# Optimization experiments

Measured on AMD Instinct MI355X. Metric: run time of the kernel, lower is better.

Reference implementation:

```python
import jax, jax.numpy as jnp
import numpy as np

N_NODES = 100000
N_EDGES = 1600000
IN_FEATS = 128
H_FEATS = 128


def setup_inputs() -> dict:
    key = jax.random.key(0)
    ks = jax.random.split(key, 8)
    s_in = 1.0 / np.sqrt(IN_FEATS)
    s_h = 1.0 / np.sqrt(H_FEATS)
    return {
        "emb_weight": jax.random.normal(ks[0], (N_NODES, IN_FEATS), jnp.float32),
        "W1_self": jax.random.normal(ks[1], (IN_FEATS, H_FEATS), jnp.float32) * s_in,
        "W1_neigh": jax.random.normal(ks[2], (IN_FEATS, H_FEATS), jnp.float32) * s_in,
        "b1": jnp.zeros((H_FEATS,), jnp.float32),
        "W2_self": jax.random.normal(ks[3], (H_FEATS, H_FEATS), jnp.float32) * s_h,
        "W2_neigh": jax.random.normal(ks[4], (H_FEATS, H_FEATS), jnp.float32) * s_h,
        "b2": jnp.zeros((H_FEATS,), jnp.float32),
        "edges": jax.random.randint(ks[5], (2, N_EDGES), 0, N_NODES, jnp.int64)
            if jax.config.jax_enable_x64 else
            jax.random.randint(ks[5], (2, N_EDGES), 0, N_NODES, jnp.int32),
    }


def _sage_conv(h, src, dst, W_self, W_neigh, b):
    # DGL SAGEConv(mean): out = h @ W_self + mean_neigh(h) @ W_neigh + b
    agg = jax.ops.segment_sum(h[src], dst, num_segments=N_NODES)  # [N, F]
    deg = jax.ops.segment_sum(jnp.ones((src.shape[0],), h.dtype), dst,
                              num_segments=N_NODES)
    mean = agg / jnp.maximum(deg, 1.0)[:, None]  # zero-in-degree -> zeros
    return h @ W_self + mean @ W_neigh + b


def reference(emb_weight, W1_self, W1_neigh, b1, W2_self, W2_neigh, b2, edges):
    src, dst = edges[0], edges[1]
    h = emb_weight  # node_emb(g.nodes()) over all nodes
    h = _sage_conv(h, src, dst, W1_self, W1_neigh, b1)
    h = jax.nn.leaky_relu(h, negative_slope=0.2)
    # dropout is identity in eval mode
    h = _sage_conv(h, src, dst, W2_self, W2_neigh, b2)
    return h
```

## Files before the change

kernel.cpp:

```cpp
#include <hip/hip_runtime.h>
#include <hip/hip_bf16.h>

#define N_NODES_C 100000
#define FEATS 128
#define SH 10
#define NBK 128
#define PB  256
#define CAST_BLOCKS 12500

typedef unsigned int uint32;
typedef __bf16 bf16_t;
typedef bf16_t bf16x8 __attribute__((ext_vector_type(8)));
typedef float f32x4 __attribute__((ext_vector_type(4)));

union Frag { uint4 u; bf16x8 v; };

__device__ __forceinline__ unsigned short f32_to_bf16_bits(float f) {
    uint32 u = __float_as_uint(f);
    u += 0x7fffu + ((u >> 16) & 1u);
    return (unsigned short)(u >> 16);
}
__device__ __forceinline__ float bf16_lo(uint32 p) { return __uint_as_float(p << 16); }
__device__ __forceinline__ float bf16_hi(uint32 p) { return __uint_as_float(p & 0xffff0000u); }

__global__ __launch_bounds__(256) void prep_fused(
    const int* __restrict__ dst, int* __restrict__ gHist, int nE, int chunk,
    const float4* __restrict__ emb4, unsigned short* __restrict__ hb0, int n4,
    const float* __restrict__ W1s, const float* __restrict__ W1n, unsigned short* __restrict__ wt1,
    const float* __restrict__ W2s, const float* __restrict__ W2n, unsigned short* __restrict__ wt2)
{
    __shared__ int h[NBK];
    const int b = blockIdx.x;
    const int tid = threadIdx.x;

    if (b < PB) {
        if (tid < NBK) h[tid] = 0;
        __syncthreads();
        const int b0 = b * chunk;
        const int e1 = min(b0 + chunk, nE);
        for (int e = b0 + tid; e < e1; e += 256)
            atomicAdd(&h[dst[e] >> SH], 1);
        __syncthreads();
        if (tid < NBK) gHist[tid * PB + b] = h[tid];
    } else if (b < PB + 32) {
        const int which = (b - PB) >> 4;
        const float* Ws = which ? W2s : W1s;
        const float* Wn = which ? W2n : W1n;
        unsigned short* wt = which ? wt2 : wt1;
        int gid = ((b - PB) & 15) * 256 + tid;
        int frag = gid >> 6, lane = gid & 63;
        int nt = frag >> 3, ks = frag & 7;
        int n = nt * 16 + (lane & 15);
        int kbase = ks * 32 + (lane >> 4) * 8;
        union { unsigned short s[8]; uint4 u; } o;
#pragma unroll
        for (int j = 0; j < 8; ++j) {
            int k = kbase + j;
            float v = (k < 128) ? Ws[(size_t)k * FEATS + n] : Wn[(size_t)(k - 128) * FEATS + n];
            o.s[j] = f32_to_bf16_bits(v);
        }
        *(uint4*)(wt + (size_t)gid * 8) = o.u;
    } else {
        int i = (b - PB - 32) * 256 + tid;
        if (i >= n4) return;
        float4 v = emb4[i];
        union { unsigned short s[4]; uint2 u; } o;
        o.s[0] = f32_to_bf16_bits(v.x);
        o.s[1] = f32_to_bf16_bits(v.y);
        o.s[2] = f32_to_bf16_bits(v.z);
        o.s[3] = f32_to_bf16_bits(v.w);
        *(uint2*)(hb0 + (size_t)i * 4) = o.u;
    }
}

__global__ __launch_bounds__(1024) void scan_one(int* __restrict__ g) {
    __shared__ int ss[1024];
    const int tid = threadIdx.x;
    const int base = tid * 32;
    int pref[32];
    int sum = 0;
#pragma unroll
    for (int j = 0; j < 32; ++j) {
        int v = g[base + j];
        pref[j] = sum;
        sum += v;
    }
    ss[tid] = sum;
    __syncthreads();
    for (int d = 1; d < 1024; d <<= 1) {
        int t = (tid >= d) ? ss[tid - d] : 0;
        __syncthreads();
        ss[tid] += t;
        __syncthreads();
    }
    int ex = ss[tid] - sum;
#pragma unroll
    for (int j = 0; j < 32; ++j)
        g[base + j] = ex + pref[j];
}

__global__ __launch_bounds__(1024) void part_scatter(const int* __restrict__ src,
                                                     const int* __restrict__ dst,
                                                     const int* __restrict__ gScan,
                                                     uint32* __restrict__ ebuf,
                                                     int nE, int chunk) {
    __shared__ int cur[NBK];
    const int tid = threadIdx.x;
    if (tid < NBK) cur[tid] = gScan[tid * PB + blockIdx.x];
    __syncthreads();
    const int b0 = blockIdx.x * chunk;
    const int e1 = min(b0 + chunk, nE);
    for (int e = b0 + tid; e < e1; e += 1024) {
        int d = dst[e];
        int pos = atomicAdd(&cur[d >> SH], 1);
        ebuf[pos] = (uint32)src[e] | ((uint32)(d & ((1 << SH) - 1)) << 17);
    }
}

__global__ __launch_bounds__(1024) void bucket_csr(const uint32* __restrict__ ebuf,
                                                   const int* __restrict__ gScan,
                                                   int* __restrict__ off,
                                                   int* __restrict__ csr,
                                                   int nE) {
    __shared__ int cnt[1 << SH];
    __shared__ int ss[1 << SH];
    const int b = blockIdx.x;
    const int tid = threadIdx.x;
    const int start = gScan[b * PB];
    const int end = gScan[(b + 1) * PB];
    const int nodeBase = b << SH;
    cnt[tid] = 0;
    __syncthreads();
    for (int e = start + tid; e < end; e += 1024)
        atomicAdd(&cnt[ebuf[e] >> 17], 1);
    __syncthreads();
    int own = cnt[tid];
    ss[tid] = own;
    __syncthreads();
    for (int d = 1; d < 1024; d <<= 1) {
        int t = (tid >= d) ? ss[tid - d] : 0;
        __syncthreads();
        ss[tid] += t;
        __syncthreads();
    }
    int ex = ss[tid] - own;
    cnt[tid] = ex;
    int node = nodeBase + tid;
    if (node < N_NODES_C) off[node] = start + ex;
    if (b == gridDim.x - 1 && tid == 0) off[N_NODES_C] = nE;
    __syncthreads();
    for (int e = start + tid; e < end; e += 1024) {
        uint32 p = ebuf[e];
        int pos = atomicAdd(&cnt[p >> 17], 1);
        csr[start + pos] = (int)((p & 0x1FFFFu) << 8);
    }
}

__global__ __launch_bounds__(256) void gather_mean_w2(const unsigned short* __restrict__ hb,
                                                      const int* __restrict__ csrB,
                                                      const int* __restrict__ off,
                                                      unsigned short* __restrict__ meanb,
                                                      int nNodes) {
    const int node = blockIdx.x * 4 + (threadIdx.x >> 6);
    const int lane = threadIdx.x & 63;
    if (node >= nNodes) return;
    const int start = __builtin_amdgcn_readfirstlane(off[node]);
    const int end   = __builtin_amdgcn_readfirstlane(off[node + 1]);
    const int half = lane >> 5;
    const int c = lane & 31;
    const char* base = (const char*)hb + (size_t)(c * 8);
    float a0 = 0.f, a1 = 0.f, a2 = 0.f, a3 = 0.f;
    int e = start;
    for (; e + 16 <= end; e += 16) {
        const int o0  = csrB[e + 0],  o1  = csrB[e + 1],  o2  = csrB[e + 2],  o3  = csrB[e + 3];
        const int o4  = csrB[e + 4],  o5  = csrB[e + 5],  o6  = csrB[e + 6],  o7  = csrB[e + 7];
        const int o8  = csrB[e + 8],  o9  = csrB[e + 9],  o10 = csrB[e + 10], o11 = csrB[e + 11];
        const int o12 = csrB[e + 12], o13 = csrB[e + 13], o14 = csrB[e + 14], o15 = csrB[e + 15];
        const uint2 u0 = *(const uint2*)(base + (size_t)(half ? o1  : o0));
        const uint2 u1 = *(const uint2*)(base + (size_t)(half ? o3  : o2));
        const uint2 u2 = *(const uint2*)(base + (size_t)(half ? o5  : o4));
        const uint2 u3 = *(const uint2*)(base + (size_t)(half ? o7  : o6));
        const uint2 u4 = *(const uint2*)(base + (size_t)(half ? o9  : o8));
        const uint2 u5 = *(const uint2*)(base + (size_t)(half ? o11 : o10));
        const uint2 u6 = *(const uint2*)(base + (size_t)(half ? o13 : o12));
        const uint2 u7 = *(const uint2*)(base + (size_t)(half ? o15 : o14));
        a0 += bf16_lo(u0.x); a1 += bf16_hi(u0.x); a2 += bf16_lo(u0.y); a3 += bf16_hi(u0.y);
        a0 += bf16_lo(u1.x); a1 += bf16_hi(u1.x); a2 += bf16_lo(u1.y); a3 += bf16_hi(u1.y);
        a0 += bf16_lo(u2.x); a1 += bf16_hi(u2.x); a2 += bf16_lo(u2.y); a3 += bf16_hi(u2.y);
        a0 += bf16_lo(u3.x); a1 += bf16_hi(u3.x); a2 += bf16_lo(u3.y); a3 += bf16_hi(u3.y);
        a0 += bf16_lo(u4.x); a1 += bf16_hi(u4.x); a2 += bf16_lo(u4.y); a3 += bf16_hi(u4.y);
        a0 += bf16_lo(u5.x); a1 += bf16_hi(u5.x); a2 += bf16_lo(u5.y); a3 += bf16_hi(u5.y);
        a0 += bf16_lo(u6.x); a1 += bf16_hi(u6.x); a2 += bf16_lo(u6.y); a3 += bf16_hi(u6.y);
        a0 += bf16_lo(u7.x); a1 += bf16_hi(u7.x); a2 += bf16_lo(u7.y); a3 += bf16_hi(u7.y);
    }
    if (e + 8 <= end) {
        const int o0 = csrB[e + 0], o1 = csrB[e + 1], o2 = csrB[e + 2], o3 = csrB[e + 3];
        const int o4 = csrB[e + 4], o5 = csrB[e + 5], o6 = csrB[e + 6], o7 = csrB[e + 7];
        const uint2 u0 = *(const uint2*)(base + (size_t)(half ? o1 : o0));
        const uint2 u1 = *(const uint2*)(base + (size_t)(half ? o3 : o2));
        const uint2 u2 = *(const uint2*)(base + (size_t)(half ? o5 : o4));
        const uint2 u3 = *(const uint2*)(base + (size_t)(half ? o7 : o6));
        a0 += bf16_lo(u0.x); a1 += bf16_hi(u0.x); a2 += bf16_lo(u0.y); a3 += bf16_hi(u0.y);
        a0 += bf16_lo(u1.x); a1 += bf16_hi(u1.x); a2 += bf16_lo(u1.y); a3 += bf16_hi(u1.y);
        a0 += bf16_lo(u2.x); a1 += bf16_hi(u2.x); a2 += bf16_lo(u2.y); a3 += bf16_hi(u2.y);
        a0 += bf16_lo(u3.x); a1 += bf16_hi(u3.x); a2 += bf16_lo(u3.y); a3 += bf16_hi(u3.y);
        e += 8;
    }
    if (e + 4 <= end) {
        const int o0 = csrB[e + 0], o1 = csrB[e + 1], o2 = csrB[e + 2], o3 = csrB[e + 3];
        const uint2 u0 = *(const uint2*)(base + (size_t)(half ? o1 : o0));
        const uint2 u1 = *(const uint2*)(base + (size_t)(half ? o3 : o2));
        a0 += bf16_lo(u0.x); a1 += bf16_hi(u0.x); a2 += bf16_lo(u0.y); a3 += bf16_hi(u0.y);
        a0 += bf16_lo(u1.x); a1 += bf16_hi(u1.x); a2 += bf16_lo(u1.y); a3 += bf16_hi(u1.y);
        e += 4;
    }
    if (e + 2 <= end) {
        const int o0 = csrB[e + 0], o1 = csrB[e + 1];
        const uint2 u = *(const uint2*)(base + (size_t)(half ? o1 : o0));
        a0 += bf16_lo(u.x); a1 += bf16_hi(u.x); a2 += bf16_lo(u.y); a3 += bf16_hi(u.y);
        e += 2;
    }
    if (e < end && half == 0) {
        const uint2 u = *(const uint2*)(base + (size_t)csrB[e]);
        a0 += bf16_lo(u.x); a1 += bf16_hi(u.x); a2 += bf16_lo(u.y); a3 += bf16_hi(u.y);
    }
    a0 += __shfl_xor(a0, 32);
    a1 += __shfl_xor(a1, 32);
    a2 += __shfl_xor(a2, 32);
    a3 += __shfl_xor(a3, 32);
    const int deg = end - start;
    const float invd = (deg > 0) ? (1.f / (float)deg) : 0.f;
    if (half == 0) {
        uint2 o;
        o.x = ((uint32)f32_to_bf16_bits(a1 * invd) << 16) | (uint32)f32_to_bf16_bits(a0 * invd);
        o.y = ((uint32)f32_to_bf16_bits(a3 * invd) << 16) | (uint32)f32_to_bf16_bits(a2 * invd);
        ((uint2*)meanb)[(size_t)node * 32 + c] = o;
    }
}

__global__ __launch_bounds__(256) void sage_gemm_mfma(const unsigned short* __restrict__ HB,
                                                      const unsigned short* __restrict__ MB,
                                                      const unsigned short* __restrict__ WT,
                                                      const float* __restrict__ bias,
                                                      void* __restrict__ OUTP,
                                                      int nNodes, int mode) {
    const int wave = threadIdx.x >> 6;
    const int lane = threadIdx.x & 63;
    const int waveBase = blockIdx.x * 64 + wave * 16;
    const int m = lane & 15;
    const int quad = lane >> 4;

    int arow = waveBase + m;
    if (arow >= nNodes) arow = nNodes - 1;
    const uint4* hrow = (const uint4*)(HB + (size_t)arow * FEATS);
    const uint4* mrow = (const uint4*)(MB + (size_t)arow * FEATS);

    Frag a[8];
#pragma unroll
    for (int ks = 0; ks < 4; ++ks) a[ks].u = hrow[ks * 4 + quad];
#pragma unroll
    for (int ks = 0; ks < 4; ++ks) a[ks + 4].u = mrow[ks * 4 + quad];

    const uint4* wt4 = (const uint4*)WT;
    f32x4 acc[8];
#pragma unroll
    for (int nt = 0; nt < 8; ++nt) acc[nt] = (f32x4){0.f, 0.f, 0.f, 0.f};

#pragma unroll
    for (int ks = 0; ks < 8; ++ks) {
#pragma unroll
        for (int nt = 0; nt < 8; ++nt) {
            Frag b;
            b.u = wt4[(size_t)(nt * 8 + ks) * 64 + lane];
            acc[nt] = __builtin_amdgcn_mfma_f32_16x16x32_bf16(a[ks].v, b.v, acc[nt], 0, 0, 0);
        }
    }

#pragma unroll
    for (int nt = 0; nt < 8; ++nt) {
        const int col = nt * 16 + m;
        const float bv = bias[col];
#pragma unroll
        for (int r = 0; r < 4; ++r) {
            const int grow = waveBase + quad * 4 + r;
            if (grow >= nNodes) continue;
            float v = acc[nt][r] + bv;
            if (mode) {
                v = v > 0.f ? v : 0.2f * v;
                ((unsigned short*)OUTP)[(size_t)grow * FEATS + col] = f32_to_bf16_bits(v);
            } else {
                ((float*)OUTP)[(size_t)grow * FEATS + col] = v;
            }
        }
    }
}

extern "C" void kernel_launch(void* const* d_in, const int* in_sizes, int n_in,
                              void* d_out, int out_size, void* d_ws, size_t ws_size,
                              hipStream_t stream) {
    const float* emb = (const float*)d_in[0];
    const float* W1s = (const float*)d_in[1];
    const float* W1n = (const float*)d_in[2];
    const float* b1  = (const float*)d_in[3];
    const float* W2s = (const float*)d_in[4];
    const float* W2n = (const float*)d_in[5];
    const float* b2  = (const float*)d_in[6];
    const int*   edg = (const int*)d_in[7];

    const int nE = in_sizes[7] / 2;
    const int* src = edg;
    const int* dst = edg + nE;

    const int chunk = (nE + PB - 1) / PB;
    const int nActB = (N_NODES_C + (1 << SH) - 1) >> SH;
    const int n4 = N_NODES_C * FEATS / 4;

    const size_t bfTab = (size_t)N_NODES_C * FEATS * sizeof(unsigned short);

    char* ws = (char*)d_ws;
    int* off      = (int*)(ws);
    int* gHist    = (int*)(ws + (512 << 10));
    int* csr      = (int*)(ws + (1 << 20));
    uint32* ebuf  = (uint32*)(ws + (8 << 20));
    unsigned short* wt1 = (unsigned short*)(ws + (15 << 20));
    unsigned short* wt2 = (unsigned short*)(ws + (15 << 20) + (64 << 10));
    unsigned short* hb0 = (unsigned short*)(ws + (16 << 20));
    unsigned short* h1b = (unsigned short*)((char*)hb0 + bfTab);
    unsigned short* mnb = (unsigned short*)((char*)h1b + bfTab);
    float* out = (float*)d_out;

    prep_fused<<<PB + 32 + CAST_BLOCKS, 256, 0, stream>>>(
        dst, gHist, nE, chunk, (const float4*)emb, hb0, n4,
        W1s, W1n, wt1, W2s, W2n, wt2);

    scan_one<<<1, 1024, 0, stream>>>(gHist);
    part_scatter<<<PB, 1024, 0, stream>>>(src, dst, gHist, ebuf, nE, chunk);
    bucket_csr<<<nActB, 1024, 0, stream>>>(ebuf, gHist, off, csr, nE);

    const int gatherBlocks = (N_NODES_C + 3) / 4;
    const int gemmBlocks = (N_NODES_C + 63) / 64;

    gather_mean_w2<<<gatherBlocks, 256, 0, stream>>>(hb0, csr, off, mnb, N_NODES_C);
    sage_gemm_mfma<<<gemmBlocks, 256, 0, stream>>>(hb0, mnb, wt1, b1, h1b, N_NODES_C, 1);

    gather_mean_w2<<<gatherBlocks, 256, 0, stream>>>(h1b, csr, off, mnb, N_NODES_C);
    sage_gemm_mfma<<<gemmBlocks, 256, 0, stream>>>(h1b, mnb, wt2, b2, out, N_NODES_C, 0);
}
```

Before: 336.1 us.

## Build CSR with per-node atomic counting and stage GEMM weights in LDS

```diff
diff --git a/kernel.cpp b/kernel.cpp
--- a/kernel.cpp
+++ b/kernel.cpp
@@ -3,8 +3,6 @@
 
 #define N_NODES_C 100000
 #define FEATS 128
-#define SH 10
-#define NBK 128
 #define PB  256
 #define CAST_BLOCKS 12500
 
@@ -24,24 +22,19 @@
 __device__ __forceinline__ float bf16_hi(uint32 p) { return __uint_as_float(p & 0xffff0000u); }
 
 __global__ __launch_bounds__(256) void prep_fused(
-    const int* __restrict__ dst, int* __restrict__ gHist, int nE, int chunk,
+    const int* __restrict__ dst, int* __restrict__ deg, int nE, int chunk,
     const float4* __restrict__ emb4, unsigned short* __restrict__ hb0, int n4,
     const float* __restrict__ W1s, const float* __restrict__ W1n, unsigned short* __restrict__ wt1,
     const float* __restrict__ W2s, const float* __restrict__ W2n, unsigned short* __restrict__ wt2)
 {
-    __shared__ int h[NBK];
     const int b = blockIdx.x;
     const int tid = threadIdx.x;
 
     if (b < PB) {
-        if (tid < NBK) h[tid] = 0;
-        __syncthreads();
         const int b0 = b * chunk;
         const int e1 = min(b0 + chunk, nE);
         for (int e = b0 + tid; e < e1; e += 256)
-            atomicAdd(&h[dst[e] >> SH], 1);
-        __syncthreads();
-        if (tid < NBK) gHist[tid * PB + b] = h[tid];
+            atomicAdd(&deg[dst[e]], 1);
     } else if (b < PB + 32) {
         const int which = (b - PB) >> 4;
         const float* Ws = which ? W2s : W1s;
@@ -73,18 +66,17 @@
     }
 }
 
-__global__ __launch_bounds__(1024) void scan_one(int* __restrict__ g) {
+__global__ __launch_bounds__(1024) void scan_nodes(const int* __restrict__ deg,
+                                                   int* __restrict__ off,
+                                                   int* __restrict__ cur,
+                                                   int nNodes, int nE) {
     __shared__ int ss[1024];
     const int tid = threadIdx.x;
-    const int base = tid * 32;
-    int pref[32];
+    const int per = (nNodes + 1023) >> 10;
+    const int lo = tid * per;
+    const int hi = min(lo + per, nNodes);
     int sum = 0;
-#pragma unroll
-    for (int j = 0; j < 32; ++j) {
-        int v = g[base + j];
-        pref[j] = sum;
-        sum += v;
-    }
+    for (int i = lo; i < hi; ++i) sum += deg[i];
     ss[tid] = sum;
     __syncthreads();
     for (int d = 1; d < 1024; d <<= 1) {
@@ -93,66 +85,25 @@
         ss[tid] += t;
         __syncthreads();
     }
-    int ex = ss[tid] - sum;
-#pragma unroll
-    for (int j = 0; j < 32; ++j)
-        g[base + j] = ex + pref[j];
-}
-
-__global__ __launch_bounds__(1024) void part_scatter(const int* __restrict__ src,
-                                                     const int* __restrict__ dst,
-                                                     const int* __restrict__ gScan,
-                                                     uint32* __restrict__ ebuf,
-                                                     int nE, int chunk) {
-    __shared__ int cur[NBK];
-    const int tid = threadIdx.x;
-    if (tid < NBK) cur[tid] = gScan[tid * PB + blockIdx.x];
-    __syncthreads();
-    const int b0 = blockIdx.x * chunk;
-    const int e1 = min(b0 + chunk, nE);
-    for (int e = b0 + tid; e < e1; e += 1024) {
-        int d = dst[e];
-        int pos = atomicAdd(&cur[d >> SH], 1);
-        ebuf[pos] = (uint32)src[e] | ((uint32)(d & ((1 << SH) - 1)) << 17);
-    }
-}
-
-__global__ __launch_bounds__(1024) void bucket_csr(const uint32* __restrict__ ebuf,
-                                                   const int* __restrict__ gScan,
-                                                   int* __restrict__ off,
+    int run = ss[tid] - sum;
+    for (int i = lo; i < hi; ++i) {
+        int d = deg[i];
+        off[i] = run;
+        cur[i] = run;
+        run += d;
+    }
+    if (tid == 0) off[nNodes] = nE;
+}
+
+__global__ __launch_bounds__(256) void place_edges(const int* __restrict__ src,
+                                                   const int* __restrict__ dst,
+                                                   int* __restrict__ cur,
                                                    int* __restrict__ csr,
                                                    int nE) {
-    __shared__ int cnt[1 << SH];
-    __shared__ int ss[1 << SH];
-    const int b = blockIdx.x;
-    const int tid = threadIdx.x;
-    const int start = gScan[b * PB];
-    const int end = gScan[(b + 1) * PB];
-    const int nodeBase = b << SH;
-    cnt[tid] = 0;
-    __syncthreads();
-    for (int e = start + tid; e < end; e += 1024)
-        atomicAdd(&cnt[ebuf[e] >> 17], 1);
-    __syncthreads();
-    int own = cnt[tid];
-    ss[tid] = own;
-    __syncthreads();
-    for (int d = 1; d < 1024; d <<= 1) {
-        int t = (tid >= d) ? ss[tid - d] : 0;
-        __syncthreads();
-        ss[tid] += t;
-        __syncthreads();
-    }
-    int ex = ss[tid] - own;
-    cnt[tid] = ex;
-    int node = nodeBase + tid;
-    if (node < N_NODES_C) off[node] = start + ex;
-    if (b == gridDim.x - 1 && tid == 0) off[N_NODES_C] = nE;
-    __syncthreads();
-    for (int e = start + tid; e < end; e += 1024) {
-        uint32 p = ebuf[e];
-        int pos = atomicAdd(&cnt[p >> 17], 1);
-        csr[start + pos] = (int)((p & 0x1FFFFu) << 8);
+    const int stride = gridDim.x * 256;
+    for (int e = blockIdx.x * 256 + threadIdx.x; e < nE; e += stride) {
+        int pos = atomicAdd(&cur[dst[e]], 1);
+        csr[pos] = src[e] << 8;
     }
 }
 
@@ -238,15 +189,22 @@
     }
 }
 
-__global__ __launch_bounds__(256) void sage_gemm_mfma(const unsigned short* __restrict__ HB,
+__global__ __launch_bounds__(512) void sage_gemm_mfma(const unsigned short* __restrict__ HB,
                                                       const unsigned short* __restrict__ MB,
                                                       const unsigned short* __restrict__ WT,
                                                       const float* __restrict__ bias,
                                                       void* __restrict__ OUTP,
                                                       int nNodes, int mode) {
-    const int wave = threadIdx.x >> 6;
-    const int lane = threadIdx.x & 63;
-    const int waveBase = blockIdx.x * 64 + wave * 16;
+    __shared__ uint4 wtl[4096];
+    const int tid = threadIdx.x;
+    const uint4* wt4 = (const uint4*)WT;
+#pragma unroll
+    for (int i = 0; i < 8; ++i)
+        wtl[i * 512 + tid] = wt4[i * 512 + tid];
+
+    const int wave = tid >> 6;
+    const int lane = tid & 63;
+    const int waveBase = blockIdx.x * 128 + wave * 16;
     const int m = lane & 15;
     const int quad = lane >> 4;
 
@@ -261,7 +219,8 @@
 #pragma unroll
     for (int ks = 0; ks < 4; ++ks) a[ks + 4].u = mrow[ks * 4 + quad];
 
-    const uint4* wt4 = (const uint4*)WT;
+    __syncthreads();
+
     f32x4 acc[8];
 #pragma unroll
     for (int nt = 0; nt < 8; ++nt) acc[nt] = (f32x4){0.f, 0.f, 0.f, 0.f};
@@ -271,7 +230,7 @@
 #pragma unroll
         for (int nt = 0; nt < 8; ++nt) {
             Frag b;
-            b.u = wt4[(size_t)(nt * 8 + ks) * 64 + lane];
+            b.u = wtl[(nt * 8 + ks) * 64 + lane];
             acc[nt] = __builtin_amdgcn_mfma_f32_16x16x32_bf16(a[ks].v, b.v, acc[nt], 0, 0, 0);
         }
     }
@@ -312,37 +271,37 @@
     const int* dst = edg + nE;
 
     const int chunk = (nE + PB - 1) / PB;
-    const int nActB = (N_NODES_C + (1 << SH) - 1) >> SH;
     const int n4 = N_NODES_C * FEATS / 4;
 
     const size_t bfTab = (size_t)N_NODES_C * FEATS * sizeof(unsigned short);
 
     char* ws = (char*)d_ws;
-    int* off      = (int*)(ws);
-    int* gHist    = (int*)(ws + (512 << 10));
-    int* csr      = (int*)(ws + (1 << 20));
-    uint32* ebuf  = (uint32*)(ws + (8 << 20));
-    unsigned short* wt1 = (unsigned short*)(ws + (15 << 20));
-    unsigned short* wt2 = (unsigned short*)(ws + (15 << 20) + (64 << 10));
+    int* off = (int*)(ws);
+    int* deg = (int*)(ws + (512 << 10));
+    int* cur = (int*)(ws + (1 << 20));
+    int* csr = (int*)(ws + (2 << 20));
+    unsigned short* wt1 = (unsigned short*)(ws + (9 << 20));
+    unsigned short* wt2 = (unsigned short*)(ws + (9 << 20) + (64 << 10));
     unsigned short* hb0 = (unsigned short*)(ws + (16 << 20));
     unsigned short* h1b = (unsigned short*)((char*)hb0 + bfTab);
     unsigned short* mnb = (unsigned short*)((char*)h1b + bfTab);
     float* out = (float*)d_out;
 
+    hipMemsetAsync(deg, 0, (size_t)N_NODES_C * sizeof(int), stream);
+
     prep_fused<<<PB + 32 + CAST_BLOCKS, 256, 0, stream>>>(
-        dst, gHist, nE, chunk, (const float4*)emb, hb0, n4,
+        dst, deg, nE, chunk, (const float4*)emb, hb0, n4,
         W1s, W1n, wt1, W2s, W2n, wt2);
 
-    scan_one<<<1, 1024, 0, stream>>>(gHist);
-    part_scatter<<<PB, 1024, 0, stream>>>(src, dst, gHist, ebuf, nE, chunk);
-    bucket_csr<<<nActB, 1024, 0, stream>>>(ebuf, gHist, off, csr, nE);
+    scan_nodes<<<1, 1024, 0, stream>>>(deg, off, cur, N_NODES_C, nE);
+    place_edges<<<2048, 256, 0, stream>>>(src, dst, cur, csr, nE);
 
     const int gatherBlocks = (N_NODES_C + 3) / 4;
-    const int gemmBlocks = (N_NODES_C + 63) / 64;
+    const int gemmBlocks = (N_NODES_C + 127) / 128;
 
     gather_mean_w2<<<gatherBlocks, 256, 0, stream>>>(hb0, csr, off, mnb, N_NODES_C);
-    sage_gemm_mfma<<<gemmBlocks, 256, 0, stream>>>(hb0, mnb, wt1, b1, h1b, N_NODES_C, 1);
+    sage_gemm_mfma<<<gemmBlocks, 512, 0, stream>>>(hb0, mnb, wt1, b1, h1b, N_NODES_C, 1);
 
     gather_mean_w2<<<gatherBlocks, 256, 0, stream>>>(h1b, csr, off, mnb, N_NODES_C);
-    sage_gemm_mfma<<<gemmBlocks, 256, 0, stream>>>(h1b, mnb, wt2, b2, out, N_NODES_C, 0);
-}
+    sage_gemm_mfma<<<gemmBlocks, 512, 0, stream>>>(h1b, mnb, wt2, b2, out, N_NODES_C, 0);
+}
```

Result: slower. 671.1 us (+99.7%).

## Stage GEMM weights in LDS with larger blocks; use finer 512-node buckets

Applied to the files above, without the earlier changes.

```diff
diff --git a/kernel.cpp b/kernel.cpp
--- a/kernel.cpp
+++ b/kernel.cpp
@@ -3,8 +3,8 @@
 
 #define N_NODES_C 100000
 #define FEATS 128
-#define SH 10
-#define NBK 128
+#define SH 9
+#define NBK 256
 #define PB  256
 #define CAST_BLOCKS 12500
 
@@ -34,14 +34,14 @@
     const int tid = threadIdx.x;
 
     if (b < PB) {
-        if (tid < NBK) h[tid] = 0;
+        h[tid] = 0;
         __syncthreads();
         const int b0 = b * chunk;
         const int e1 = min(b0 + chunk, nE);
         for (int e = b0 + tid; e < e1; e += 256)
             atomicAdd(&h[dst[e] >> SH], 1);
         __syncthreads();
-        if (tid < NBK) gHist[tid * PB + b] = h[tid];
+        gHist[tid * PB + b] = h[tid];
     } else if (b < PB + 32) {
         const int which = (b - PB) >> 4;
         const float* Ws = which ? W2s : W1s;
@@ -76,11 +76,11 @@
 __global__ __launch_bounds__(1024) void scan_one(int* __restrict__ g) {
     __shared__ int ss[1024];
     const int tid = threadIdx.x;
-    const int base = tid * 32;
-    int pref[32];
+    const int base = tid * 64;
+    int pref[64];
     int sum = 0;
 #pragma unroll
-    for (int j = 0; j < 32; ++j) {
+    for (int j = 0; j < 64; ++j) {
         int v = g[base + j];
         pref[j] = sum;
         sum += v;
@@ -95,7 +95,7 @@
     }
     int ex = ss[tid] - sum;
 #pragma unroll
-    for (int j = 0; j < 32; ++j)
+    for (int j = 0; j < 64; ++j)
         g[base + j] = ex + pref[j];
 }
 
@@ -129,24 +129,27 @@
     const int start = gScan[b * PB];
     const int end = gScan[(b + 1) * PB];
     const int nodeBase = b << SH;
-    cnt[tid] = 0;
+    if (tid < (1 << SH)) cnt[tid] = 0;
     __syncthreads();
     for (int e = start + tid; e < end; e += 1024)
         atomicAdd(&cnt[ebuf[e] >> 17], 1);
     __syncthreads();
-    int own = cnt[tid];
-    ss[tid] = own;
-    __syncthreads();
-    for (int d = 1; d < 1024; d <<= 1) {
-        int t = (tid >= d) ? ss[tid - d] : 0;
-        __syncthreads();
-        ss[tid] += t;
-        __syncthreads();
-    }
-    int ex = ss[tid] - own;
-    cnt[tid] = ex;
-    int node = nodeBase + tid;
-    if (node < N_NODES_C) off[node] = start + ex;
+    int own = 0;
+    if (tid < (1 << SH)) { own = cnt[tid]; ss[tid] = own; }
+    __syncthreads();
+    for (int d = 1; d < (1 << SH); d <<= 1) {
+        int t = 0;
+        if (tid < (1 << SH) && tid >= d) t = ss[tid - d];
+        __syncthreads();
+        if (tid < (1 << SH)) ss[tid] += t;
+        __syncthreads();
+    }
+    if (tid < (1 << SH)) {
+        int ex = ss[tid] - own;
+        cnt[tid] = ex;
+        int node = nodeBase + tid;
+        if (node < N_NODES_C) off[node] = start + ex;
+    }
     if (b == gridDim.x - 1 && tid == 0) off[N_NODES_C] = nE;
     __syncthreads();
     for (int e = start + tid; e < end; e += 1024) {
@@ -238,15 +241,22 @@
     }
 }
 
-__global__ __launch_bounds__(256) void sage_gemm_mfma(const unsigned short* __restrict__ HB,
+__global__ __launch_bounds__(512) void sage_gemm_mfma(const unsigned short* __restrict__ HB,
                                                       const unsigned short* __restrict__ MB,
                                                       const unsigned short* __restrict__ WT,
                                                       const float* __restrict__ bias,
                                                       void* __restrict__ OUTP,
                                                       int nNodes, int mode) {
-    const int wave = threadIdx.x >> 6;
-    const int lane = threadIdx.x & 63;
-    const int waveBase = blockIdx.x * 64 + wave * 16;
+    __shared__ uint4 wtl[4096];
+    const int tid = threadIdx.x;
+    const uint4* wt4 = (const uint4*)WT;
+#pragma unroll
+    for (int i = 0; i < 8; ++i)
+        wtl[i * 512 + tid] = wt4[i * 512 + tid];
+
+    const int wave = tid >> 6;
+    const int lane = tid & 63;
+    const int waveBase = blockIdx.x * 128 + wave * 16;
     const int m = lane & 15;
     const int quad = lane >> 4;
 
@@ -261,7 +271,8 @@
 #pragma unroll
     for (int ks = 0; ks < 4; ++ks) a[ks + 4].u = mrow[ks * 4 + quad];
 
-    const uint4* wt4 = (const uint4*)WT;
+    __syncthreads();
+
     f32x4 acc[8];
 #pragma unroll
     for (int nt = 0; nt < 8; ++nt) acc[nt] = (f32x4){0.f, 0.f, 0.f, 0.f};
@@ -271,7 +282,7 @@
 #pragma unroll
         for (int nt = 0; nt < 8; ++nt) {
             Frag b;
-            b.u = wt4[(size_t)(nt * 8 + ks) * 64 + lane];
+            b.u = wtl[(nt * 8 + ks) * 64 + lane];
             acc[nt] = __builtin_amdgcn_mfma_f32_16x16x32_bf16(a[ks].v, b.v, acc[nt], 0, 0, 0);
         }
     }
@@ -338,11 +349,11 @@
     bucket_csr<<<nActB, 1024, 0, stream>>>(ebuf, gHist, off, csr, nE);
 
     const int gatherBlocks = (N_NODES_C + 3) / 4;
-    const int gemmBlocks = (N_NODES_C + 63) / 64;
+    const int gemmBlocks = (N_NODES_C + 127) / 128;
 
     gather_mean_w2<<<gatherBlocks, 256, 0, stream>>>(hb0, csr, off, mnb, N_NODES_C);
-    sage_gemm_mfma<<<gemmBlocks, 256, 0, stream>>>(hb0, mnb, wt1, b1, h1b, N_NODES_C, 1);
+    sage_gemm_mfma<<<gemmBlocks, 512, 0, stream>>>(hb0, mnb, wt1, b1, h1b, N_NODES_C, 1);
 
     gather_mean_w2<<<gatherBlocks, 256, 0, stream>>>(h1b, csr, off, mnb, N_NODES_C);
-    sage_gemm_mfma<<<gemmBlocks, 256, 0, stream>>>(h1b, mnb, wt2, b2, out, N_NODES_C, 0);
-}
+    sage_gemm_mfma<<<gemmBlocks, 512, 0, stream>>>(h1b, mnb, wt2, b2, out, N_NODES_C, 0);
+}
```

New measurement: 329.2 us. 1.02x faster.
